# Kernel tuning notes

Hardware: AMD Instinct MI355X
Metric: run time of the kernel (lower is better)

The kernel has to match this reference:

```python
import jax, jax.numpy as jnp
import numpy as np
from jax import lax

C = 256
EPS = 1e-5
DN = ('NCHW', 'OIHW', 'NCHW')


def dw_conv(x, w, dilation):
    # depthwise conv, groups=C, stride 1, 'same' padding for odd kernels
    K = w.shape[2]
    pad = dilation * (K - 1) // 2
    return lax.conv_general_dilated(
        x, w, window_strides=(1, 1), padding=[(pad, pad), (pad, pad)],
        rhs_dilation=(dilation, dilation), dimension_numbers=DN,
        feature_group_count=C)


def batchnorm(y, gamma, beta):
    # training-mode BN: batch stats over (N,H,W), biased variance (torch semantics)
    m = jnp.mean(y, axis=(0, 2, 3), keepdims=True)
    v = jnp.mean((y - m) ** 2, axis=(0, 2, 3), keepdims=True)
    g = gamma.reshape(1, C, 1, 1)
    b = beta.reshape(1, C, 1, 1)
    return (y - m) * (g * lax.rsqrt(v + EPS)) + b


def setup_inputs() -> dict:
    key = jax.random.key(0)
    ks = jax.random.split(key, 20)
    d = {
        'x': jax.random.normal(ks[0], (8, C, 112, 112), jnp.float32),
        'w_origin': jax.random.normal(ks[1], (C, 1, 11, 11), jnp.float32) * 0.05,
        'g_origin': jax.random.uniform(ks[2], (C,), jnp.float32, 0.5, 1.5),
        'b_origin': jax.random.normal(ks[3], (C,), jnp.float32) * 0.05,
    }
    branches = [('k5_1', 5), ('k7_1', 7), ('k5_2', 5), ('k3_3', 3), ('k3_5', 3)]
    i = 4
    for name, K in branches:
        d[f'w_{name}'] = jax.random.normal(ks[i], (C, 1, K, K), jnp.float32) * 0.05
        d[f'g_{name}'] = jax.random.uniform(ks[i + 1], (C,), jnp.float32, 0.5, 1.5)
        d[f'b_{name}'] = jax.random.normal(ks[i + 2], (C,), jnp.float32) * 0.05
        i += 3
    return d


def reference(x, w_origin, g_origin, b_origin,
              w_k5_1, g_k5_1, b_k5_1,
              w_k7_1, g_k7_1, b_k7_1,
              w_k5_2, g_k5_2, b_k5_2,
              w_k3_3, g_k3_3, b_k3_3,
              w_k3_5, g_k3_5, b_k3_5):
    out = batchnorm(dw_conv(x, w_origin, 1), g_origin, b_origin)
    branches = [
        (w_k5_1, g_k5_1, b_k5_1, 1),
        (w_k7_1, g_k7_1, b_k7_1, 1),
        (w_k5_2, g_k5_2, b_k5_2, 2),
        (w_k3_3, g_k3_3, b_k3_3, 3),
        (w_k3_5, g_k3_5, b_k3_5, 5),
    ]
    for w, g, b, r in branches:
        out = out + batchnorm(dw_conv(x, w, r), g, b)
    return out
```

## Files before the change

### kernel.cpp

```cpp
#include <hip/hip_runtime.h>
#include <math.h>

#define NCH   256
#define HH    112
#define WW    112
#define NB    8
#define PLANE (HH*WW)
#define LSTR  132
#define LOFF  9
#define COLG  (WW/8)
#define ROWS_PER 56
#define TROWS 66
#define NTASK (ROWS_PER*COLG)
#define BNEPS 1e-5f

template<int K, int DIL>
__device__ __forceinline__ void branch_row(float acc[8], const float* __restrict__ wc,
                                           const int dy, const float xr[20]) {
  constexpr int P = (K - 1) / 2;
  if (dy % DIL != 0) return;
  const int q = dy / DIL;
  if (q < -P || q > P) return;
  const float* wrow = wc + (q + P) * K;
  #pragma unroll
  for (int kj = 0; kj < K; ++kj) {
    const float wv = wrow[kj];
    const int off = 5 + (kj - P) * DIL;
    #pragma unroll
    for (int j = 0; j < 8; ++j)
      acc[j] = fmaf(wv, xr[j + off], acc[j]);
  }
}

__device__ __forceinline__ void load_half_to_lds(float* tile, const float* __restrict__ x,
                                                 int plane, int r0, int tid) {
  float4* t4 = reinterpret_cast<float4*>(tile);
  #pragma unroll 2
  for (int i = tid; i < TROWS * LSTR / 4; i += 256) t4[i] = make_float4(0.f, 0.f, 0.f, 0.f);
  __syncthreads();
  const float* xp = x + (size_t)plane * PLANE;
  for (int i = tid; i < TROWS * (WW / 4); i += 256) {
    const int tr = i / (WW / 4);
    const int c4 = (i - tr * (WW / 4)) * 4;
    const int ir = r0 - 5 + tr;
    if (ir >= 0 && ir < HH) {
      const float4 v = *reinterpret_cast<const float4*>(xp + ir * WW + c4);
      float* d = &tile[tr * LSTR + LOFF + c4];
      d[0] = v.x; d[1] = v.y; d[2] = v.z; d[3] = v.w;
    }
  }
  __syncthreads();
}

__device__ __forceinline__ void read_row20(float xr[20], const float* base) {
  const float4* lp = reinterpret_cast<const float4*>(base);
  #pragma unroll
  for (int q = 0; q < 5; ++q) {
    const float4 v = lp[q];
    xr[4 * q] = v.x; xr[4 * q + 1] = v.y; xr[4 * q + 2] = v.z; xr[4 * q + 3] = v.w;
  }
}

extern "C" __global__ void __launch_bounds__(256, 4)
k_stats(const float* __restrict__ x,
        const float* __restrict__ w0, const float* __restrict__ w1,
        const float* __restrict__ w2, const float* __restrict__ w3,
        const float* __restrict__ w4, const float* __restrict__ w5,
        float* __restrict__ partials)
{
  __shared__ __align__(16) float tile[TROWS * LSTR];
  const int bid   = blockIdx.x;
  const int plane = bid >> 1;
  const int r0    = (bid & 1) * ROWS_PER;
  const int ch    = plane & (NCH - 1);
  const int tid   = threadIdx.x;

  load_half_to_lds(tile, x, plane, r0, tid);

  const float* wc0 = w0 + ch * 121;
  const float* wc1 = w1 + ch * 25;
  const float* wc2 = w2 + ch * 49;
  const float* wc3 = w3 + ch * 25;
  const float* wc4 = w4 + ch * 9;
  const float* wc5 = w5 + ch * 9;

  float s[6]  = {0.f, 0.f, 0.f, 0.f, 0.f, 0.f};
  float ss[6] = {0.f, 0.f, 0.f, 0.f, 0.f, 0.f};

  for (int t = tid; t < NTASK; t += 256) {
    const int rl = t % ROWS_PER;
    const int c0 = (t / ROWS_PER) * 8;
    const float* base = &tile[(rl + 5) * LSTR + c0 + 4];
    float acc[6][8];
    #pragma unroll
    for (int b = 0; b < 6; ++b) {
      #pragma unroll
      for (int j = 0; j < 8; ++j) acc[b][j] = 0.f;
    }
    #pragma unroll
    for (int dy = -5; dy <= 5; ++dy) {
      float xr[20];
      read_row20(xr, base + dy * LSTR);
      branch_row<11, 1>(acc[0], wc0, dy, xr);
      branch_row< 5, 1>(acc[1], wc1, dy, xr);
      branch_row< 7, 1>(acc[2], wc2, dy, xr);
      branch_row< 5, 2>(acc[3], wc3, dy, xr);
      branch_row< 3, 3>(acc[4], wc4, dy, xr);
      branch_row< 3, 5>(acc[5], wc5, dy, xr);
    }
    #pragma unroll
    for (int b = 0; b < 6; ++b) {
      #pragma unroll
      for (int j = 0; j < 8; ++j) { const float v = acc[b][j]; s[b] += v; ss[b] += v * v; }
    }
  }

  __syncthreads();
  #pragma unroll
  for (int b = 0; b < 6; ++b) {
    #pragma unroll
    for (int off = 32; off > 0; off >>= 1) {
      s[b]  += __shfl_xor(s[b],  off, 64);
      ss[b] += __shfl_xor(ss[b], off, 64);
    }
  }
  const int lane = tid & 63, wid = tid >> 6;
  if (lane == 0) {
    #pragma unroll
    for (int b = 0; b < 6; ++b) { tile[wid * 12 + 2 * b] = s[b]; tile[wid * 12 + 2 * b + 1] = ss[b]; }
  }
  __syncthreads();
  if (tid < 12) {
    partials[(size_t)bid * 12 + tid] =
        tile[tid] + tile[12 + tid] + tile[24 + tid] + tile[36 + tid];
  }
}

template<int K, int DIL>
__device__ __forceinline__ void merge_k(float* wmv, const float* __restrict__ wc, const float sc) {
  constexpr int P = (K - 1) / 2;
  #pragma unroll
  for (int ki = 0; ki < K; ++ki) {
    #pragma unroll
    for (int kj = 0; kj < K; ++kj) {
      const int idx = ((ki - P) * DIL + 5) * 11 + ((kj - P) * DIL + 5);
      wmv[idx] += sc * wc[ki * K + kj];
    }
  }
}

extern "C" __global__ void __launch_bounds__(256)
k_merge(const float* __restrict__ partials,
        const float* __restrict__ w0, const float* __restrict__ g0, const float* __restrict__ b0,
        const float* __restrict__ w1, const float* __restrict__ g1, const float* __restrict__ b1,
        const float* __restrict__ w2, const float* __restrict__ g2, const float* __restrict__ b2,
        const float* __restrict__ w3, const float* __restrict__ g3, const float* __restrict__ b3,
        const float* __restrict__ w4, const float* __restrict__ g4, const float* __restrict__ b4,
        const float* __restrict__ w5, const float* __restrict__ g5, const float* __restrict__ b5,
        float* __restrict__ wm, float* __restrict__ bias)
{
  const int ch = threadIdx.x;
  const float invc = 1.f / (float)(NB * PLANE);
  float wmv[121];
  #pragma unroll
  for (int i = 0; i < 121; ++i) wmv[i] = 0.f;
  float bacc = 0.f;

#define BR_STATS(B)                                                                 \
    float S = 0.f, SS = 0.f;                                                        \
    for (int n = 0; n < NB; ++n) {                                                  \
      for (int h = 0; h < 2; ++h) {                                                 \
        const float* p = &partials[(size_t)((n * NCH + ch) * 2 + h) * 12 + 2 * (B)];\
        S += p[0]; SS += p[1];                                                      \
      }                                                                             \
    }                                                                               \
    const float m = S * invc;                                                       \
    const float v = fmaxf(SS * invc - m * m, 0.f);

  { BR_STATS(0) const float sc = g0[ch] / sqrtf(v + BNEPS); bacc += b0[ch] - m * sc; merge_k<11, 1>(wmv, w0 + ch * 121, sc); }
  { BR_STATS(1) const float sc = g1[ch] / sqrtf(v + BNEPS); bacc += b1[ch] - m * sc; merge_k< 5, 1>(wmv, w1 + ch * 25,  sc); }
  { BR_STATS(2) const float sc = g2[ch] / sqrtf(v + BNEPS); bacc += b2[ch] - m * sc; merge_k< 7, 1>(wmv, w2 + ch * 49,  sc); }
  { BR_STATS(3) const float sc = g3[ch] / sqrtf(v + BNEPS); bacc += b3[ch] - m * sc; merge_k< 5, 2>(wmv, w3 + ch * 25,  sc); }
  { BR_STATS(4) const float sc = g4[ch] / sqrtf(v + BNEPS); bacc += b4[ch] - m * sc; merge_k< 3, 3>(wmv, w4 + ch * 9,   sc); }
  { BR_STATS(5) const float sc = g5[ch] / sqrtf(v + BNEPS); bacc += b5[ch] - m * sc; merge_k< 3, 5>(wmv, w5 + ch * 9,   sc); }
#undef BR_STATS

  #pragma unroll
  for (int i = 0; i < 121; ++i) wm[(size_t)ch * 121 + i] = wmv[i];
  bias[ch] = bacc;
}

extern "C" __global__ void __launch_bounds__(256, 4)
k_conv(const float* __restrict__ x, const float* __restrict__ wm,
       const float* __restrict__ bias, float* __restrict__ out)
{
  __shared__ __align__(16) float tile[TROWS * LSTR];
  const int bid   = blockIdx.x;
  const int plane = bid >> 1;
  const int r0    = (bid & 1) * ROWS_PER;
  const int ch    = plane & (NCH - 1);
  const int tid   = threadIdx.x;

  load_half_to_lds(tile, x, plane, r0, tid);

  const float* wmc = wm + (size_t)ch * 121;
  const float bc   = bias[ch];
  float* op = out + (size_t)plane * PLANE;

  for (int t = tid; t < NTASK; t += 256) {
    const int rl = t / COLG;
    const int c0 = (t - rl * COLG) * 8;
    const float* base = &tile[(rl + 5) * LSTR + c0 + 4];
    float acc[8];
    #pragma unroll
    for (int j = 0; j < 8; ++j) acc[j] = bc;

    #pragma unroll
    for (int dy = -5; dy <= 5; ++dy) {
      float xr[20];
      read_row20(xr, base + dy * LSTR);
      const float* wrow = wmc + (dy + 5) * 11;
      #pragma unroll
      for (int kj = 0; kj < 11; ++kj) {
        const float wv = wrow[kj];
        #pragma unroll
        for (int j = 0; j < 8; ++j) acc[j] = fmaf(wv, xr[j + kj], acc[j]);
      }
    }
    float4 o0 = make_float4(acc[0], acc[1], acc[2], acc[3]);
    float4 o1 = make_float4(acc[4], acc[5], acc[6], acc[7]);
    float* dst = &op[(r0 + rl) * WW + c0];
    reinterpret_cast<float4*>(dst)[0] = o0;
    reinterpret_cast<float4*>(dst)[1] = o1;
  }
}

extern "C" void kernel_launch(void* const* d_in, const int* in_sizes, int n_in,
                              void* d_out, int out_size, void* d_ws, size_t ws_size,
                              hipStream_t stream) {
  (void)in_sizes; (void)n_in; (void)out_size; (void)ws_size;
  const float* x   = (const float*)d_in[0];
  const float* w0  = (const float*)d_in[1];
  const float* g0  = (const float*)d_in[2];
  const float* b0  = (const float*)d_in[3];
  const float* w1  = (const float*)d_in[4];
  const float* g1  = (const float*)d_in[5];
  const float* b1  = (const float*)d_in[6];
  const float* w2  = (const float*)d_in[7];
  const float* g2  = (const float*)d_in[8];
  const float* b2  = (const float*)d_in[9];
  const float* w3  = (const float*)d_in[10];
  const float* g3  = (const float*)d_in[11];
  const float* b3  = (const float*)d_in[12];
  const float* w4  = (const float*)d_in[13];
  const float* g4  = (const float*)d_in[14];
  const float* b4  = (const float*)d_in[15];
  const float* w5  = (const float*)d_in[16];
  const float* g5  = (const float*)d_in[17];
  const float* b5  = (const float*)d_in[18];

  float* partials = (float*)d_ws;
  float* wm       = partials + 4096 * 12;
  float* bias     = wm + 256 * 121;
  float* outp     = (float*)d_out;

  k_stats<<<dim3(NB * NCH * 2), dim3(256), 0, stream>>>(x, w0, w1, w2, w3, w4, w5, partials);
  k_merge<<<dim3(1), dim3(256), 0, stream>>>(partials,
      w0, g0, b0, w1, g1, b1, w2, g2, b2, w3, g3, b3, w4, g4, b4, w5, g5, b5,
      wm, bias);
  k_conv<<<dim3(NB * NCH * 2), dim3(256), 0, stream>>>(x, wm, bias, outp);
}
```

Measured before the change: 446.2 us.

## Split stats kernel into two branch passes and compute two rows per thread in conv

The stats kernel now runs two separate passes of three branches each. The second pass covers only dy in [-4,4], so it skips row reads the smaller kernels never need, and each pass keeps fewer accumulators live, which lowers register pressure. The conv kernel gives each thread two adjacent output rows, so each of the 12 LDS row reads feeds both accumulators and LDS traffic per output drops. The cost is two loops over the tile in the stats kernel and more live registers in the conv kernel.

```diff
diff --git a/kernel.cpp b/kernel.cpp
--- a/kernel.cpp
+++ b/kernel.cpp
@@ -12,6 +12,7 @@
 #define ROWS_PER 56
 #define TROWS 66
 #define NTASK (ROWS_PER*COLG)
+#define CTASK ((ROWS_PER/2)*COLG)
 #define BNEPS 1e-5f
 
 template<int K, int DIL>
@@ -61,6 +62,38 @@
   }
 }
 
+template<int K0,int D0,int K1,int D1,int K2,int D2,int DYLO,int DYHI>
+__device__ __forceinline__ void stats_pass(const float* __restrict__ tile, int tid,
+    const float* __restrict__ wa, const float* __restrict__ wb,
+    const float* __restrict__ wc,
+    float* s0p, float* ss0p, float* s1p, float* ss1p, float* s2p, float* ss2p)
+{
+  float s0 = 0.f, ss0 = 0.f, s1 = 0.f, ss1 = 0.f, s2 = 0.f, ss2 = 0.f;
+  for (int t = tid; t < NTASK; t += 256) {
+    const int rl = t % ROWS_PER;
+    const int c0 = (t / ROWS_PER) * 8;
+    const float* base = &tile[(rl + 5) * LSTR + c0 + 4];
+    float a0[8], a1[8], a2[8];
+    #pragma unroll
+    for (int j = 0; j < 8; ++j) { a0[j] = 0.f; a1[j] = 0.f; a2[j] = 0.f; }
+    #pragma unroll
+    for (int dy = DYLO; dy <= DYHI; ++dy) {
+      float xr[20];
+      read_row20(xr, base + dy * LSTR);
+      branch_row<K0, D0>(a0, wa, dy, xr);
+      branch_row<K1, D1>(a1, wb, dy, xr);
+      branch_row<K2, D2>(a2, wc, dy, xr);
+    }
+    #pragma unroll
+    for (int j = 0; j < 8; ++j) {
+      s0 += a0[j]; ss0 = fmaf(a0[j], a0[j], ss0);
+      s1 += a1[j]; ss1 = fmaf(a1[j], a1[j], ss1);
+      s2 += a2[j]; ss2 = fmaf(a2[j], a2[j], ss2);
+    }
+  }
+  *s0p = s0; *ss0p = ss0; *s1p = s1; *ss1p = ss1; *s2p = s2; *ss2p = ss2;
+}
+
 extern "C" __global__ void __launch_bounds__(256, 4)
 k_stats(const float* __restrict__ x,
         const float* __restrict__ w0, const float* __restrict__ w1,
@@ -77,43 +110,13 @@
 
   load_half_to_lds(tile, x, plane, r0, tid);
 
-  const float* wc0 = w0 + ch * 121;
-  const float* wc1 = w1 + ch * 25;
-  const float* wc2 = w2 + ch * 49;
-  const float* wc3 = w3 + ch * 25;
-  const float* wc4 = w4 + ch * 9;
-  const float* wc5 = w5 + ch * 9;
-
-  float s[6]  = {0.f, 0.f, 0.f, 0.f, 0.f, 0.f};
-  float ss[6] = {0.f, 0.f, 0.f, 0.f, 0.f, 0.f};
-
-  for (int t = tid; t < NTASK; t += 256) {
-    const int rl = t % ROWS_PER;
-    const int c0 = (t / ROWS_PER) * 8;
-    const float* base = &tile[(rl + 5) * LSTR + c0 + 4];
-    float acc[6][8];
-    #pragma unroll
-    for (int b = 0; b < 6; ++b) {
-      #pragma unroll
-      for (int j = 0; j < 8; ++j) acc[b][j] = 0.f;
-    }
-    #pragma unroll
-    for (int dy = -5; dy <= 5; ++dy) {
-      float xr[20];
-      read_row20(xr, base + dy * LSTR);
-      branch_row<11, 1>(acc[0], wc0, dy, xr);
-      branch_row< 5, 1>(acc[1], wc1, dy, xr);
-      branch_row< 7, 1>(acc[2], wc2, dy, xr);
-      branch_row< 5, 2>(acc[3], wc3, dy, xr);
-      branch_row< 3, 3>(acc[4], wc4, dy, xr);
-      branch_row< 3, 5>(acc[5], wc5, dy, xr);
-    }
-    #pragma unroll
-    for (int b = 0; b < 6; ++b) {
-      #pragma unroll
-      for (int j = 0; j < 8; ++j) { const float v = acc[b][j]; s[b] += v; ss[b] += v * v; }
-    }
-  }
+  float s[6], ss[6];
+  stats_pass<11,1, 3,3, 3,5, -5,5>(tile, tid,
+      w0 + ch * 121, w4 + ch * 9, w5 + ch * 9,
+      &s[0], &ss[0], &s[4], &ss[4], &s[5], &ss[5]);
+  stats_pass< 5,1, 7,1, 5,2, -4,4>(tile, tid,
+      w1 + ch * 25, w2 + ch * 49, w3 + ch * 25,
+      &s[1], &ss[1], &s[2], &ss[2], &s[3], &ss[3]);
 
   __syncthreads();
   #pragma unroll
@@ -207,31 +210,43 @@
   const float bc   = bias[ch];
   float* op = out + (size_t)plane * PLANE;
 
-  for (int t = tid; t < NTASK; t += 256) {
-    const int rl = t / COLG;
-    const int c0 = (t - rl * COLG) * 8;
-    const float* base = &tile[(rl + 5) * LSTR + c0 + 4];
-    float acc[8];
-    #pragma unroll
-    for (int j = 0; j < 8; ++j) acc[j] = bc;
-
-    #pragma unroll
-    for (int dy = -5; dy <= 5; ++dy) {
+  for (int t = tid; t < CTASK; t += 256) {
+    const int rg = t / COLG;
+    const int c0 = (t - rg * COLG) * 8;
+    const float* base = &tile[(2 * rg) * LSTR + c0 + 4];
+    float a0[8], a1[8];
+    #pragma unroll
+    for (int j = 0; j < 8; ++j) { a0[j] = bc; a1[j] = bc; }
+
+    #pragma unroll
+    for (int d = 0; d < 12; ++d) {
       float xr[20];
-      read_row20(xr, base + dy * LSTR);
-      const float* wrow = wmc + (dy + 5) * 11;
-      #pragma unroll
-      for (int kj = 0; kj < 11; ++kj) {
-        const float wv = wrow[kj];
+      read_row20(xr, base + d * LSTR);
+      if (d < 11) {
+        const float* wr = wmc + d * 11;
         #pragma unroll
-        for (int j = 0; j < 8; ++j) acc[j] = fmaf(wv, xr[j + kj], acc[j]);
+        for (int kj = 0; kj < 11; ++kj) {
+          const float wv = wr[kj];
+          #pragma unroll
+          for (int j = 0; j < 8; ++j) a0[j] = fmaf(wv, xr[j + kj], a0[j]);
+        }
       }
-    }
-    float4 o0 = make_float4(acc[0], acc[1], acc[2], acc[3]);
-    float4 o1 = make_float4(acc[4], acc[5], acc[6], acc[7]);
-    float* dst = &op[(r0 + rl) * WW + c0];
-    reinterpret_cast<float4*>(dst)[0] = o0;
-    reinterpret_cast<float4*>(dst)[1] = o1;
+      if (d >= 1) {
+        const float* wr = wmc + (d - 1) * 11;
+        #pragma unroll
+        for (int kj = 0; kj < 11; ++kj) {
+          const float wv = wr[kj];
+          #pragma unroll
+          for (int j = 0; j < 8; ++j) a1[j] = fmaf(wv, xr[j + kj], a1[j]);
+        }
+      }
+    }
+    float* dst0 = &op[(r0 + 2 * rg) * WW + c0];
+    float* dst1 = dst0 + WW;
+    reinterpret_cast<float4*>(dst0)[0] = make_float4(a0[0], a0[1], a0[2], a0[3]);
+    reinterpret_cast<float4*>(dst0)[1] = make_float4(a0[4], a0[5], a0[6], a0[7]);
+    reinterpret_cast<float4*>(dst1)[0] = make_float4(a1[0], a1[1], a1[2], a1[3]);
+    reinterpret_cast<float4*>(dst1)[1] = make_float4(a1[4], a1[5], a1[6], a1[7]);
   }
 }
 
```

New measurement: 443.4 us. No clear change (-0.6%).
